# Kernel optimization log

Hardware: AMD Instinct MI355X
Metric: run time of the kernel (lower is better)

## Reference

```python
import jax, jax.numpy as jnp
import numpy as np

B, S, D, H = 4, 256, 128, 8
HD = D // H          # head_dim = 16
DD = D // 2          # desc dim = 64 (required: 2*DD == H*HD for edge_type='normal')
T = S + 1            # new_seq (CLS + variables)
NEG_INF = -1e9


def setup_inputs() -> dict:
    key = jax.random.key(0)
    ks = jax.random.split(key, 8)
    p = lambda k, shape: jax.random.normal(k, shape, dtype=jnp.float32) * 0.05
    return {
        "desc_embeddings": jax.random.normal(ks[0], (B, S, DD), dtype=jnp.float32),
        "name_value_embeddings": jax.random.normal(ks[1], (B, T, D), dtype=jnp.float32),
        "Wq": p(ks[2], (D, D)), "bq": jnp.zeros((D,), jnp.float32),
        "Wk": p(ks[3], (D, D)), "bk": jnp.zeros((D,), jnp.float32),
        "Wv": p(ks[4], (D, D)), "bv": jnp.zeros((D,), jnp.float32),
        "aw": p(ks[5], (3 * HD,)),               # attn_proj weight (Linear(3*head_dim, 1))
        "ab": jnp.zeros((), jnp.float32),         # attn_proj bias
    }


def reference(desc_embeddings, name_value_embeddings, Wq, bq, Wk, bk, Wv, bv, aw, ab):
    # Projections -> [B, H, T, HD]
    def proj(W, b):
        y = name_value_embeddings @ W.T + b
        return y.reshape(B, T, H, HD).transpose(0, 2, 1, 3)
    q = proj(Wq, bq)
    k = proj(Wk, bk)
    v = proj(Wv, bv)

    # Structural adjacency: Var-Var without self loops, CLS->Var on, Var->CLS off.
    var_adj = 1.0 - jnp.eye(S, dtype=jnp.float32)          # no_self_loop=True
    adj = jnp.zeros((T, T), jnp.float32)
    adj = adj.at[1:, 1:].set(var_adj).at[0, 1:].set(1.0)   # [T, T], same for all batches

    # Edge attributes: e[b,i,j] = [desc_i, desc_j] on Var-Var block; [desc, desc] on CLS row/col.
    de = desc_embeddings                                    # [B, S, DD]
    edge = jnp.zeros((B, T, T, 2 * DD), jnp.float32)
    edge = edge.at[:, 1:, 1:, :DD].set(de[:, :, None, :])
    edge = edge.at[:, 1:, 1:, DD:].set(de[:, None, :, :])
    cls_e = jnp.concatenate([de, de], axis=-1)              # [B, S, 2*DD]
    edge = edge.at[:, 0, 1:, :].set(cls_e).at[:, 1:, 0, :].set(cls_e)
    eh = edge.reshape(B, T, T, H, HD)                       # per-head edge features

    # attn_proj(cat([q_i, k_j, e_ij])) decomposes linearly (gat_v1: no nonlinearity before):
    # score = q_i.aq + k_j.ak + (adj * e_ij).ae + bias   (edge masked by adjacency pre-linear)
    aq, ak, ae = aw[:HD], aw[HD:2 * HD], aw[2 * HD:]
    sq = jnp.einsum('bhid,d->bhi', q, aq)                   # [B, H, T]
    sk = jnp.einsum('bhjd,d->bhj', k, ak)
    se = jnp.einsum('bijhd,d->bhij', eh, ae) * adj[None, None, :, :]
    logits = sq[:, :, :, None] + sk[:, :, None, :] + se + ab

    # Masked softmax (struct mask as additive -1e9 where adjacency == 0)
    logits = logits + jnp.where(adj == 0.0, NEG_INF, 0.0)[None, None, :, :]
    attn = jax.nn.softmax(logits, axis=-1)                  # [B, H, T, T]; dropout is eval-mode identity

    ctx = jnp.einsum('bhij,bhjd->bhid', attn, v)            # [B, H, T, HD]
    basis_outputs = ctx.transpose(0, 2, 1, 3)               # [B, T, H, HD]
    return basis_outputs, attn
```

## Files before the change

### kernel.cpp

```cpp
#include <hip/hip_runtime.h>

#define NB 4
#define SS 256
#define DM 128
#define NH 8
#define HD 16
#define DDim 64
#define TT 257
#define NPOS (NB*TT)

#define OFF_SQ  2080
#define OFF_SK  10304
#define OFF_G   18528
#define OFF_V   22640
#define ATT_BASE (NB*TT*NH*HD)

#define DPPF(x, ctrl) __int_as_float(__builtin_amdgcn_update_dpp(0, __float_as_int(x), (ctrl), 0xf, 0xf, true))
#define SWZF(x, off)  __int_as_float(__builtin_amdgcn_ds_swizzle(__float_as_int(x), (off)))

__device__ __forceinline__ float wred_max(float x) {
  x = fmaxf(x, DPPF(x, 0xB1));
  x = fmaxf(x, DPPF(x, 0x4E));
  x = fmaxf(x, DPPF(x, 0x141));
  x = fmaxf(x, DPPF(x, 0x140));
  x = fmaxf(x, SWZF(x, 0x401F));
  x = fmaxf(x, __shfl_xor(x, 32));
  return x;
}
__device__ __forceinline__ float wred_sum(float x) {
  x += DPPF(x, 0xB1);
  x += DPPF(x, 0x4E);
  x += DPPF(x, 0x141);
  x += DPPF(x, 0x140);
  x += SWZF(x, 0x401F);
  x += __shfl_xor(x, 32);
  return x;
}
__device__ __forceinline__ float red_jj(float x) {
  x += DPPF(x, 0x124);
  x += DPPF(x, 0x128);
  x += SWZF(x, 0x401F);
  x += __shfl_xor(x, 32);
  return x;
}

__global__ __launch_bounds__(256) void proj_kernel(
    const float* __restrict__ de, const float* __restrict__ nve,
    const float* __restrict__ Wq, const float* __restrict__ bq,
    const float* __restrict__ Wk, const float* __restrict__ bk,
    const float* __restrict__ Wv, const float* __restrict__ bv,
    const float* __restrict__ aw, float* __restrict__ ws)
{
  __shared__ float4 xs4[4][32];
  int tid = threadIdx.x;
  int pos0 = blockIdx.x * 4;
  if (tid < 128) {
    int lp = tid >> 5, e4 = tid & 31;
    xs4[lp][e4] = ((const float4*)nve)[(pos0 + lp)*32 + e4];
  }
  __syncthreads();

  int c = tid & 127, ph = tid >> 7;
  int dd = c & 15, h = c >> 4;
  const float4* wq4 = (const float4*)(Wq + c*DM);
  const float4* wk4 = (const float4*)(Wk + c*DM);
  const float4* wv4 = (const float4*)(Wv + c*DM);
  float aqd = aw[dd], akd = aw[16 + dd];

  float accq[2] = {bq[c], bq[c]};
  float acck[2] = {bk[c], bk[c]};
  float accv[2] = {bv[c], bv[c]};

  #pragma unroll 4
  for (int e4 = 0; e4 < 32; ++e4) {
    float4 wq = wq4[e4], wk = wk4[e4], wv = wv4[e4];
    #pragma unroll
    for (int p = 0; p < 2; ++p) {
      float4 x = xs4[ph*2 + p][e4];
      accq[p] += wq.x*x.x + wq.y*x.y + wq.z*x.z + wq.w*x.w;
      acck[p] += wk.x*x.x + wk.y*x.y + wk.z*x.z + wk.w*x.w;
      accv[p] += wv.x*x.x + wv.y*x.y + wv.z*x.z + wv.w*x.w;
    }
  }

  #pragma unroll
  for (int p = 0; p < 2; ++p) {
    int pos = pos0 + ph*2 + p;
    int b = pos / TT, t = pos - b*TT;
    ws[OFF_V + ((b*NH + h)*TT + t)*HD + dd] = accv[p];
    float vq = accq[p] * aqd, vk = acck[p] * akd;
    vq += __shfl_xor(vq, 1); vq += __shfl_xor(vq, 2);
    vq += __shfl_xor(vq, 4); vq += __shfl_xor(vq, 8);
    vk += __shfl_xor(vk, 1); vk += __shfl_xor(vk, 2);
    vk += __shfl_xor(vk, 4); vk += __shfl_xor(vk, 8);
    if (dd == 0) {
      ws[OFF_SQ + (b*NH + h)*TT + t] = vq;
      ws[OFF_SK + (b*NH + h)*TT + t] = vk;
    }
  }

  if (tid < 16) {
    int gi = blockIdx.x * 16 + tid;
    int bm = gi / TT, t = gi - bm*TT;
    float val = 0.f;
    if (t > 0) {
      int b = bm >> 2, m = bm & 3;
      const float* dp = de + (b*SS + (t-1))*DDim + m*16;
      #pragma unroll
      for (int d = 0; d < 16; ++d) val += dp[d] * aw[32 + d];
    }
    ws[OFF_G + gi] = val;
  }
}

__global__ __launch_bounds__(256) void attn_kernel(
    const float* __restrict__ ws, const float* __restrict__ ab_ptr,
    float* __restrict__ out)
{
  __shared__ float4 v_lds[272*4];
  __shared__ float4 p4_lds[4][272];
  __shared__ float u_lds[260];
  __shared__ float g_lds[260];

  int tid  = threadIdx.x;
  int wave = tid >> 6, lane = tid & 63;
  int rb = blockIdx.x % 17;
  int bh = blockIdx.x / 17;
  int h = bh & 7, b = bh >> 3;
  bool hge = (h >= 4);

  const float4* v4 = (const float4*)(ws + OFF_V + bh*TT*HD);
  const float* skp = ws + OFF_SK + bh*TT;
  const float* gp  = ws + OFF_G + (b*4 + (h & 3))*TT;
  for (int idx = tid; idx < 272*4; idx += 256)
    v_lds[idx] = (idx < TT*4) ? v4[idx] : make_float4(0.f,0.f,0.f,0.f);
  for (int j = tid; j < 260; j += 256) {
    float g = (j < TT) ? gp[j]  : 0.f;
    float u = (j < TT) ? skp[j] : 0.f;
    u_lds[j] = u + (hge ? g : 0.f);
    g_lds[j] = g;
  }
  __syncthreads();

  float ab = ab_ptr[0];
  int i0 = rb*16 + wave*4;
  bool ext0 = (i0 == 0) && !hge;

  float Ci[4]; bool valid[4];
  #pragma unroll
  for (int r = 0; r < 4; ++r) {
    int i = i0 + r;
    valid[r] = (i < TT);
    int ic = valid[r] ? i : 256;
    Ci[r] = ws[OFF_SQ + bh*TT + ic] + ab;
    if (!hge && i > 0) Ci[r] += g_lds[ic];
  }

  float l[4][4];
  float mx[4] = {-3.0e38f, -3.0e38f, -3.0e38f, -3.0e38f};
  #pragma unroll
  for (int k = 0; k < 4; ++k) {
    int j = lane + 64*k;
    float base = u_lds[j];
    float gv = 0.f;
    if (ext0) gv = g_lds[j];
    #pragma unroll
    for (int r = 0; r < 4; ++r) {
      int i = i0 + r;
      float lv = Ci[r] + base;
      if (r == 0 && ext0) lv += gv;
      bool msk = (j == 0) || (i > 0 && j == i);
      l[r][k] = msk ? -3.0e38f : lv;
      mx[r] = fmaxf(mx[r], l[r][k]);
    }
  }
  float lt[4] = {-3.0e38f, -3.0e38f, -3.0e38f, -3.0e38f};
  if (lane == 0) {
    float base = u_lds[256];
    float gv = ext0 ? g_lds[256] : 0.f;
    #pragma unroll
    for (int r = 0; r < 4; ++r) {
      int i = i0 + r;
      float lv = Ci[r] + base;
      if (r == 0 && ext0) lv += gv;
      lt[r] = (i == 256) ? -3.0e38f : lv;
      mx[r] = fmaxf(mx[r], lt[r]);
    }
  }
  #pragma unroll
  for (int r = 0; r < 4; ++r) mx[r] = wred_max(mx[r]);

  float pn[4][4];
  float s[4] = {0.f,0.f,0.f,0.f};
  #pragma unroll
  for (int r = 0; r < 4; ++r) {
    #pragma unroll
    for (int k = 0; k < 4; ++k) {
      float p = __expf(l[r][k] - mx[r]);
      pn[r][k] = p;
      s[r] += p;
    }
  }
  float pt[4] = {0.f,0.f,0.f,0.f};
  if (lane == 0) {
    #pragma unroll
    for (int r = 0; r < 4; ++r) { pt[r] = __expf(lt[r] - mx[r]); s[r] += pt[r]; }
  }
  float inv[4];
  #pragma unroll
  for (int r = 0; r < 4; ++r) inv[r] = 1.0f / wred_sum(s[r]);

  #pragma unroll
  for (int k = 0; k < 4; ++k) {
    int j = lane + 64*k;
    #pragma unroll
    for (int r = 0; r < 4; ++r) {
      pn[r][k] *= inv[r];
      if (valid[r]) out[ATT_BASE + (bh*TT + (i0+r))*TT + j] = pn[r][k];
    }
    p4_lds[wave][j] = make_float4(pn[0][k], pn[1][k], pn[2][k], pn[3][k]);
  }
  if (lane == 0) {
    float4 t4;
    float* tp = (float*)&t4;
    #pragma unroll
    for (int r = 0; r < 4; ++r) {
      tp[r] = pt[r] * inv[r];
      if (valid[r]) out[ATT_BASE + (bh*TT + (i0+r))*TT + 256] = tp[r];
    }
    p4_lds[wave][256] = t4;
  }
  if (lane >= 1 && lane < 16)
    p4_lds[wave][256 + lane] = make_float4(0.f,0.f,0.f,0.f);
  __syncthreads();

  int jjlo = lane >> 2, dq = lane & 3;
  float4 acc0 = {0,0,0,0}, acc1 = {0,0,0,0}, acc2 = {0,0,0,0}, acc3 = {0,0,0,0};
  #pragma unroll
  for (int it = 0; it < 17; ++it) {
    int jj = it*16 + jjlo;
    float4 v = v_lds[jj*4 + dq];
    float4 p = p4_lds[wave][jj];
    acc0.x += p.x*v.x; acc0.y += p.x*v.y; acc0.z += p.x*v.z; acc0.w += p.x*v.w;
    acc1.x += p.y*v.x; acc1.y += p.y*v.y; acc1.z += p.y*v.z; acc1.w += p.y*v.w;
    acc2.x += p.z*v.x; acc2.y += p.z*v.y; acc2.z += p.z*v.z; acc2.w += p.z*v.w;
    acc3.x += p.w*v.x; acc3.y += p.w*v.y; acc3.z += p.w*v.z; acc3.w += p.w*v.w;
  }
  float4 accs[4] = {acc0, acc1, acc2, acc3};
  #pragma unroll
  for (int r = 0; r < 4; ++r) {
    accs[r].x = red_jj(accs[r].x);
    accs[r].y = red_jj(accs[r].y);
    accs[r].z = red_jj(accs[r].z);
    accs[r].w = red_jj(accs[r].w);
  }
  if (lane < 4) {
    #pragma unroll
    for (int r = 0; r < 4; ++r) {
      if (valid[r])
        *(float4*)(out + ((b*TT + (i0+r))*NH + h)*HD + lane*4) = accs[r];
    }
  }
}

extern "C" void kernel_launch(void* const* d_in, const int* in_sizes, int n_in,
                              void* d_out, int out_size, void* d_ws, size_t ws_size,
                              hipStream_t stream) {
  const float* de  = (const float*)d_in[0];
  const float* nve = (const float*)d_in[1];
  const float* Wq  = (const float*)d_in[2];
  const float* bq  = (const float*)d_in[3];
  const float* Wk  = (const float*)d_in[4];
  const float* bk  = (const float*)d_in[5];
  const float* Wv  = (const float*)d_in[6];
  const float* bv  = (const float*)d_in[7];
  const float* aw  = (const float*)d_in[8];
  const float* ab  = (const float*)d_in[9];
  float* out = (float*)d_out;
  float* ws  = (float*)d_ws;

  proj_kernel<<<NPOS/4, 256, 0, stream>>>(de, nve, Wq, bq, Wk, bk, Wv, bv, aw, ws);
  attn_kernel<<<32*17, 256, 0, stream>>>(ws, ab, out);
}
```

Before: 38.08 us.

## Fold attention weight vectors into Q/K projections and batch 16 positions per block

A new setup kernel precomputes Wq·aq and Wk·ak (and the matching bias dot products) as per-head 128-wide vectors, plus the edge term G. The projection kernel then computes only V and two scalar score projections per head, instead of full Q and K. It also handles 16 positions per block so each V weight load is reused more. The cost is an extra kernel launch, and the 16 extra lanes doing score dots add divergence inside the wave.

```diff
diff --git a/kernel.cpp b/kernel.cpp
--- a/kernel.cpp
+++ b/kernel.cpp
@@ -9,6 +9,10 @@
 #define TT 257
 #define NPOS (NB*TT)
 
+#define OFF_WQE 0
+#define OFF_WKE 1024
+#define OFF_BQE 2048
+#define OFF_BKE 2064
 #define OFF_SQ  2080
 #define OFF_SK  10304
 #define OFF_G   18528
@@ -44,72 +48,106 @@
   return x;
 }
 
-__global__ __launch_bounds__(256) void proj_kernel(
-    const float* __restrict__ de, const float* __restrict__ nve,
+__global__ __launch_bounds__(256) void setup_kernel(
+    const float* __restrict__ de,
     const float* __restrict__ Wq, const float* __restrict__ bq,
     const float* __restrict__ Wk, const float* __restrict__ bk,
-    const float* __restrict__ Wv, const float* __restrict__ bv,
     const float* __restrict__ aw, float* __restrict__ ws)
 {
-  __shared__ float4 xs4[4][32];
+  int tid = threadIdx.x, bid = blockIdx.x;
+  if (bid < 4) {
+    int idx = bid*256 + tid;
+    int h = idx >> 7, e = idx & 127;
+    float sq_ = 0.f, sk_ = 0.f;
+    #pragma unroll
+    for (int d = 0; d < 16; ++d) {
+      sq_ += Wq[(h*16+d)*DM + e] * aw[d];
+      sk_ += Wk[(h*16+d)*DM + e] * aw[16+d];
+    }
+    ws[OFF_WQE + idx] = sq_;
+    ws[OFF_WKE + idx] = sk_;
+    if (bid == 0 && tid < 16) {
+      int hh = tid & 7; bool isq = (tid < 8);
+      float s = 0.f;
+      #pragma unroll
+      for (int d = 0; d < 16; ++d)
+        s += isq ? bq[hh*16+d]*aw[d] : bk[hh*16+d]*aw[16+d];
+      ws[(isq ? OFF_BQE : OFF_BKE) + hh] = s;
+    }
+  } else {
+    int chunk = (bid - 4) * 1028;
+    int lim = chunk + 1028;
+    for (int r = 0; r < 5; ++r) {
+      int gi = chunk + tid + r*256;
+      if (gi < lim && gi < 16*TT) {
+        int bm = gi / TT, t = gi - bm*TT;
+        float val = 0.f;
+        if (t > 0) {
+          int b = bm >> 2, m = bm & 3;
+          const float* dp = de + (b*SS + (t-1))*DDim + m*16;
+          #pragma unroll
+          for (int d = 0; d < 16; ++d) val += dp[d] * aw[32+d];
+        }
+        ws[OFF_G + gi] = val;
+      }
+    }
+  }
+}
+
+__global__ __launch_bounds__(256) void proj_kernel(
+    const float* __restrict__ nve,
+    const float* __restrict__ Wv, const float* __restrict__ bv,
+    float* __restrict__ ws)
+{
+  __shared__ float4 xs4[16][32];
   int tid = threadIdx.x;
-  int pos0 = blockIdx.x * 4;
-  if (tid < 128) {
-    int lp = tid >> 5, e4 = tid & 31;
-    xs4[lp][e4] = ((const float4*)nve)[(pos0 + lp)*32 + e4];
+  int pos0 = blockIdx.x * 16;
+  const float4* nve4 = (const float4*)nve;
+  for (int idx = tid; idx < 512; idx += 256) {
+    int lp = idx >> 5, e4 = idx & 31;
+    int pos = pos0 + lp;
+    xs4[lp][e4] = (pos < NPOS) ? nve4[pos*32 + e4] : make_float4(0.f,0.f,0.f,0.f);
   }
   __syncthreads();
 
   int c = tid & 127, ph = tid >> 7;
-  int dd = c & 15, h = c >> 4;
-  const float4* wq4 = (const float4*)(Wq + c*DM);
-  const float4* wk4 = (const float4*)(Wk + c*DM);
   const float4* wv4 = (const float4*)(Wv + c*DM);
-  float aqd = aw[dd], akd = aw[16 + dd];
-
-  float accq[2] = {bq[c], bq[c]};
-  float acck[2] = {bk[c], bk[c]};
-  float accv[2] = {bv[c], bv[c]};
+  bool doe = (c < 16);
+  const float4* we4 = doe
+      ? (const float4*)(ws + (c < 8 ? OFF_WQE + c*DM : OFF_WKE + (c-8)*DM))
+      : wv4;
+
+  float acc[8]  = {0.f,0.f,0.f,0.f,0.f,0.f,0.f,0.f};
+  float acce[8] = {0.f,0.f,0.f,0.f,0.f,0.f,0.f,0.f};
 
   #pragma unroll 4
   for (int e4 = 0; e4 < 32; ++e4) {
-    float4 wq = wq4[e4], wk = wk4[e4], wv = wv4[e4];
-    #pragma unroll
-    for (int p = 0; p < 2; ++p) {
-      float4 x = xs4[ph*2 + p][e4];
-      accq[p] += wq.x*x.x + wq.y*x.y + wq.z*x.z + wq.w*x.w;
-      acck[p] += wk.x*x.x + wk.y*x.y + wk.z*x.z + wk.w*x.w;
-      accv[p] += wv.x*x.x + wv.y*x.y + wv.z*x.z + wv.w*x.w;
-    }
-  }
-
-  #pragma unroll
-  for (int p = 0; p < 2; ++p) {
-    int pos = pos0 + ph*2 + p;
+    float4 w = wv4[e4];
+    #pragma unroll
+    for (int p = 0; p < 8; ++p) {
+      float4 x = xs4[ph*8+p][e4];
+      acc[p] += w.x*x.x + w.y*x.y + w.z*x.z + w.w*x.w;
+    }
+    if (doe) {
+      float4 we = we4[e4];
+      #pragma unroll
+      for (int p = 0; p < 8; ++p) {
+        float4 x = xs4[ph*8+p][e4];
+        acce[p] += we.x*x.x + we.y*x.y + we.z*x.z + we.w*x.w;
+      }
+    }
+  }
+
+  int h = c >> 4, d = c & 15;
+  float bvc = bv[c];
+  float be  = doe ? ws[(c < 8 ? OFF_BQE + c : OFF_BKE + (c-8))] : 0.f;
+  for (int p = 0; p < 8; ++p) {
+    int pos = pos0 + ph*8 + p;
+    if (pos >= NPOS) break;
     int b = pos / TT, t = pos - b*TT;
-    ws[OFF_V + ((b*NH + h)*TT + t)*HD + dd] = accv[p];
-    float vq = accq[p] * aqd, vk = acck[p] * akd;
-    vq += __shfl_xor(vq, 1); vq += __shfl_xor(vq, 2);
-    vq += __shfl_xor(vq, 4); vq += __shfl_xor(vq, 8);
-    vk += __shfl_xor(vk, 1); vk += __shfl_xor(vk, 2);
-    vk += __shfl_xor(vk, 4); vk += __shfl_xor(vk, 8);
-    if (dd == 0) {
-      ws[OFF_SQ + (b*NH + h)*TT + t] = vq;
-      ws[OFF_SK + (b*NH + h)*TT + t] = vk;
-    }
-  }
-
-  if (tid < 16) {
-    int gi = blockIdx.x * 16 + tid;
-    int bm = gi / TT, t = gi - bm*TT;
-    float val = 0.f;
-    if (t > 0) {
-      int b = bm >> 2, m = bm & 3;
-      const float* dp = de + (b*SS + (t-1))*DDim + m*16;
-      #pragma unroll
-      for (int d = 0; d < 16; ++d) val += dp[d] * aw[32 + d];
-    }
-    ws[OFF_G + gi] = val;
+    ws[OFF_V + ((b*NH + h)*TT + t)*HD + d] = acc[p] + bvc;
+    if (c < 8)       ws[OFF_SQ + (b*NH + c)*TT + t]     = acce[p] + be;
+    else if (c < 16) ws[OFF_SK + (b*NH + (c-8))*TT + t] = acce[p] + be;
   }
 }
 
@@ -279,6 +317,7 @@
   float* out = (float*)d_out;
   float* ws  = (float*)d_ws;
 
-  proj_kernel<<<NPOS/4, 256, 0, stream>>>(de, nve, Wq, bq, Wk, bk, Wv, bv, aw, ws);
+  setup_kernel<<<8, 256, 0, stream>>>(de, Wq, bq, Wk, bk, aw, ws);
+  proj_kernel<<<(NPOS + 15)/16, 256, 0, stream>>>(nve, Wv, bv, ws);
   attn_kernel<<<32*17, 256, 0, stream>>>(ws, ab, out);
 }
```

After: 31.94 us. 1.19x faster.
